# Kernel optimization log

Measured on AMD Instinct MI355X. Metric: run time of the kernel, lower is better.

## Reference

```python
import jax, jax.numpy as jnp
from jax import lax
import numpy as np

V, D_EMB, H, P, B, T = 32000, 512, 1024, 512, 32, 512
NUM_LAYERS = 2


def setup_inputs() -> dict:
    key = jax.random.key(0)
    ks = jax.random.split(key, 2 + NUM_LAYERS * 5)
    tokens = jax.random.randint(ks[0], (B, T), 0, V, dtype=jnp.int32)
    embed = jax.random.normal(ks[1], (V, D_EMB), dtype=jnp.float32) * 0.02
    inp = {"tokens": tokens, "embed": embed}
    in_dims = [D_EMB] + [P] * (NUM_LAYERS - 1)
    for l in range(NUM_LAYERS):
        kk = ks[2 + 5 * l: 7 + 5 * l]
        inp[f"Wx{l}"] = jax.random.normal(kk[0], (in_dims[l], 4 * H), dtype=jnp.float32) * 0.02
        inp[f"Wh{l}"] = jax.random.normal(kk[1], (H, 4 * H), dtype=jnp.float32) * 0.02
        inp[f"b{l}"] = jnp.zeros((4 * H,), dtype=jnp.float32)
        inp[f"Wfc{l}"] = jax.random.normal(kk[3], (H, P), dtype=jnp.float32) * 0.02
        inp[f"bfc{l}"] = jnp.zeros((P,), dtype=jnp.float32)
    return inp


def _lstm(x, Wx, Wh, b):
    # x: [B, T, D] -> [B, T, H]. Keras gate order: i, f, g(cell), o.
    Bsz = x.shape[0]
    h0 = jnp.zeros((Bsz, H), dtype=x.dtype)
    c0 = jnp.zeros((Bsz, H), dtype=x.dtype)

    # Precompute input projection for all timesteps (one big GEMM).
    xz = jnp.einsum('btd,dg->btg', x, Wx) + b  # [B, T, 4H]

    def step(carry, zt):
        h, c = carry
        z = zt + h @ Wh
        i, f, g, o = jnp.split(z, 4, axis=-1)
        c = jax.nn.sigmoid(f) * c + jax.nn.sigmoid(i) * jnp.tanh(g)
        h = jax.nn.sigmoid(o) * jnp.tanh(c)
        return (h, c), h

    _, ys = lax.scan(step, (h0, c0), jnp.swapaxes(xz, 0, 1))  # ys: [T, B, H]
    return jnp.swapaxes(ys, 0, 1)


def reference(tokens, embed, Wx0, Wh0, b0, Wfc0, bfc0, Wx1, Wh1, b1, Wfc1, bfc1):
    # inference path: dropout is identity (training=False), use_softmax=False
    x = embed[tokens]  # [B, T, D_EMB]
    layers = [(Wx0, Wh0, b0, Wfc0, bfc0), (Wx1, Wh1, b1, Wfc1, bfc1)]
    for Wx, Wh, b, Wfc, bfc in layers:
        x = _lstm(x, Wx, Wh, b)
        x = x @ Wfc + bfc  # per-layer dense projection [B, T, P]
    return x
```

## Files before the change

kernel.cpp:

```cpp
#include <hip/hip_runtime.h>
#include <cstdio>
#include <cstdint>

typedef unsigned short u16;
typedef unsigned int u32;
typedef float f32x4 __attribute__((ext_vector_type(4)));
typedef short s16x8 __attribute__((ext_vector_type(8)));
typedef int i32x2 __attribute__((ext_vector_type(2)));

#define DI __device__ __forceinline__

#define BATCH 32
#define SEQT 512
#define HDIM 1024
#define PDIM 512
#define DEMB 512
#define G4H 4096

DI u16 f2bf(float f) {
  u32 u = __float_as_uint(f);
  return (u16)((u + 0x7fffu + ((u >> 16) & 1u)) >> 16);
}
DI float bf2f(u16 h) { return __uint_as_float(((u32)h) << 16); }
DI void split2(float f, u16 &hi, u16 &lo) {
  hi = f2bf(f);
  lo = f2bf(f - bf2f(hi));
}
DI f32x4 mfma16(s16x8 a, s16x8 b, f32x4 c) {
  return __builtin_amdgcn_mfma_f32_16x16x32_bf16(a, b, c, 0, 0, 0);
}
DI void dma16(const void *g, void *l) {
  __builtin_amdgcn_global_load_lds((const __attribute__((address_space(1))) void *)g,
                                   (__attribute__((address_space(3))) void *)l, 16, 0, 0);
}
DI s16x8 ld128_dev(const u16 *p) {
  s16x8 r;
  asm volatile("global_load_dwordx4 %0, %1, off sc1" : "=v"(r) : "v"(p));
  return r;
}
DI i32x2 ld64_dev(const u16 *p) {
  i32x2 r;
  asm volatile("global_load_dwordx2 %0, %1, off sc1" : "=v"(r) : "v"(p));
  return r;
}
DI void st16_dev(u16 *p, u16 v) {
  asm volatile("global_store_short %0, %1, off sc1" ::"v"(p), "v"((u32)v) : "memory");
}
DI void st32_dev(int *p, int v) {
  asm volatile("global_store_dword %0, %1, off sc1" ::"v"(p), "v"(v) : "memory");
}
DI void st64_dev(u16 *p, i32x2 v) {
  asm volatile("global_store_dwordx2 %0, %1, off sc1" ::"v"(p), "v"(v) : "memory");
}
DI u32 sentq(s16x8 v) {
  union U { s16x8 s; u32 d[4]; } u;
  u.s = v;
  u32 b = 0;
#pragma unroll
  for (int i = 0; i < 4; ++i)
    b |= (u32)(((u.d[i] & 0xffffu) == 0xffffu) || ((u.d[i] >> 16) == 0xffffu));
  return b;
}

#if __has_builtin(__builtin_amdgcn_exp2f) && __has_builtin(__builtin_amdgcn_rcpf)
DI float fsig(float x) {
  return __builtin_amdgcn_rcpf(1.f + __builtin_amdgcn_exp2f(-1.4426950408889634f * x));
}
DI float ftanh(float x) {
  return 2.f * __builtin_amdgcn_rcpf(1.f + __builtin_amdgcn_exp2f(-2.8853900817779268f * x)) - 1.f;
}
#else
DI float fsig(float x) { return 1.f / (1.f + expf(-x)); }
DI float ftanh(float x) { return tanhf(x); }
#endif

__global__ void k_gather_pack(const int *__restrict__ tokens, const float *__restrict__ embed,
                              u16 *__restrict__ xhi, u16 *__restrict__ xlo) {
  int idx = blockIdx.x * 256 + threadIdx.x;
  int m = idx >> 6;
  int k8 = (idx & 63) << 3;
  int tok = tokens[m];
  const float *src = embed + (size_t)tok * DEMB + k8;
  float4 a = *(const float4 *)src;
  float4 b = *(const float4 *)(src + 4);
  float v[8] = {a.x, a.y, a.z, a.w, b.x, b.y, b.z, b.w};
  union UV { u16 h[8]; int4 v; };
  UV uh, ul;
#pragma unroll
  for (int j = 0; j < 8; ++j) split2(v[j], uh.h[j], ul.h[j]);
  size_t o = (size_t)m * DEMB + k8;
  *(int4 *)(xhi + o) = uh.v;
  *(int4 *)(xlo + o) = ul.v;
}

__global__ void k_packT(const float *__restrict__ W, u16 *__restrict__ Thi, u16 *__restrict__ Tlo,
                        int K, int N) {
  __shared__ float tile[32][33];
  int n0 = blockIdx.x * 32, k0 = blockIdx.y * 32;
  int tx = threadIdx.x, ty = threadIdx.y;
#pragma unroll
  for (int i = 0; i < 4; ++i) tile[ty + 8 * i][tx] = W[(size_t)(k0 + ty + 8 * i) * N + n0 + tx];
  __syncthreads();
#pragma unroll
  for (int i = 0; i < 4; ++i) {
    int n = ty + 8 * i;
    u16 hi, lo;
    split2(tile[tx][n], hi, lo);
    size_t o = (size_t)(n0 + n) * K + k0 + tx;
    Thi[o] = hi;
    Tlo[o] = lo;
  }
}

__global__ void k_split(const float *__restrict__ W, u16 *__restrict__ hi, u16 *__restrict__ lo,
                        int n) {
  int i = blockIdx.x * 256 + threadIdx.x;
  if (i < n) split2(W[i], hi[i], lo[i]);
}

__global__ void k_beff(const float *__restrict__ bfc0, const float *__restrict__ Wx1,
                       const float *__restrict__ b1, float *__restrict__ beff) {
  int n = blockIdx.x * 256 + threadIdx.x;
  float acc = b1[n];
  for (int j = 0; j < PDIM; ++j) acc += bfc0[j] * Wx1[(size_t)j * G4H + n];
  beff[n] = acc;
}

template <int OM, int SA>
__global__ __launch_bounds__(256, 2) void k_gemm(const u16 *__restrict__ Ahi, const u16 *__restrict__ Alo,
                                                 const u16 *__restrict__ Bhi, const u16 *__restrict__ Blo,
                                                 const float *__restrict__ bias, void *__restrict__ out0,
                                                 int M, int N, int K) {
  __shared__ u16 sP[4][128 * 64];
  const int tid = threadIdx.x;
  const int w = tid >> 6, lane = tid & 63;
  const int la15 = lane & 15, la4 = lane >> 4;
  const int nbn = N >> 7;
  const int bm = blockIdx.x / nbn, bn = blockIdx.x % nbn;
  const u16 *src = (w == 0) ? Ahi : (w == 1) ? Alo : (w == 2) ? Bhi : Blo;
  const int rowbase = (w < 2) ? bm * 128 : bn * 128;
  char *lds = (char *)&sP[w][0];

  if (SA) {
    for (int i = tid; i < 2048; i += 256) ((unsigned long long *)&sP[1][0])[i] = 0ULL;
  }

  f32x4 acc[2][8] = {};
  for (int kb = 0; kb < K; kb += 64) {
    if (!(SA && w == 1)) {
#pragma unroll
      for (int i = 0; i < 16; ++i) {
        int s = i * 64 + lane;
        int row = s >> 3;
        int k16 = (s & 7) ^ (row & 7);
        dma16(src + (size_t)(rowbase + row) * K + kb + k16 * 8, lds + i * 1024);
      }
    }
    asm volatile("s_waitcnt vmcnt(0)" ::: "memory");
    __syncthreads();
#pragma unroll
    for (int ksl = 0; ksl < 2; ++ksl) {
      s16x8 ah[2], al[2];
#pragma unroll
      for (int rf = 0; rf < 2; ++rf) {
        int row = 32 * w + 16 * rf + la15;
        int slot = row * 8 + ((4 * ksl + la4) ^ (row & 7));
        ah[rf] = *(const s16x8 *)((const char *)&sP[0][0] + slot * 16);
        al[rf] = *(const s16x8 *)((const char *)&sP[1][0] + slot * 16);
      }
#pragma unroll
      for (int cf = 0; cf < 8; ++cf) {
        int col = 16 * cf + la15;
        int slot = col * 8 + ((4 * ksl + la4) ^ (col & 7));
        s16x8 bh = *(const s16x8 *)((const char *)&sP[2][0] + slot * 16);
        s16x8 bl = *(const s16x8 *)((const char *)&sP[3][0] + slot * 16);
#pragma unroll
        for (int rf = 0; rf < 2; ++rf) {
          acc[rf][cf] = mfma16(ah[rf], bh, acc[rf][cf]);
          acc[rf][cf] = mfma16(ah[rf], bl, acc[rf][cf]);
          acc[rf][cf] = mfma16(al[rf], bh, acc[rf][cf]);
        }
      }
    }
    __syncthreads();
  }
#pragma unroll
  for (int rf = 0; rf < 2; ++rf) {
#pragma unroll
    for (int cf = 0; cf < 8; ++cf) {
      int c = bn * 128 + 16 * cf + la15;
      float bv = bias ? bias[c] : 0.f;
#pragma unroll
      for (int q = 0; q < 4; ++q) {
        int r = bm * 128 + 32 * w + 16 * rf + 4 * la4 + q;
        float v = acc[rf][cf][q] + bv;
        if (OM == 0) {
          ((u16 *)out0)[(size_t)r * N + c] = f2bf(v);
        } else {
          int b2 = r & 31, tt = r >> 5;
          ((float *)out0)[((size_t)b2 * SEQT + tt) * PDIM + c] = v;
        }
      }
    }
  }
}

__global__ __launch_bounds__(256, 1) void k_recur_pipe(
    const u16 *__restrict__ xz0, const float *__restrict__ Wh0, const float *__restrict__ Wh1,
    const u16 *__restrict__ Weff, const float *__restrict__ beff,
    u16 *h0h, u16 *h1h, u16 *zeffR, int *flags) {
  __shared__ u16 sW[32 * 1024];
  __shared__ u16 sE[32 * 1024];
  __shared__ float zacc[4][32][33];
  __shared__ float zE[32][33];
  __shared__ float sC[256];
  const int tid = threadIdx.x;
  const int w = tid >> 6, lane = tid & 63;
  const int la15 = lane & 15, la4 = lane >> 4;
  const int wg = blockIdx.x;
  const int layer = wg >> 7;
  const int g = wg & 127;

  const float *Wh = layer ? Wh1 : Wh0;
  for (int i2 = tid; i2 < 32 * 1024; i2 += 256) {
    int zc = i2 & 31;
    int k = i2 >> 5;
    int gcol = (zc >> 3) * HDIM + 8 * g + (zc & 7);
    int boff = zc * 2048 + ((((k >> 3) ^ (zc & 7))) << 4) + (k & 7) * 2;
    *(u16 *)((char *)sW + boff) = f2bf(Wh[(size_t)k * G4H + gcol]);
    if (!layer) *(u16 *)((char *)sE + boff) = Weff[(size_t)k * G4H + gcol];
  }
  sC[tid] = 0.f;
  __syncthreads();

  const int r_g = tid >> 3, hc = tid & 7;
  const int ks0 = 8 * w;

  if (!layer) {
    for (int t = 0; t <= SEQT; ++t) {
      const bool last = (t == SEQT);
      float xzv[4] = {0.f, 0.f, 0.f, 0.f};
      if (!last) {
        const u16 *px = xz0 + ((size_t)r_g * SEQT + t) * G4H + 8 * g + hc;
#pragma unroll
        for (int gi = 0; gi < 4; ++gi) xzv[gi] = bf2f(px[(size_t)gi * HDIM]);
      }
      if (w == 0 && (t & 7) == 0 && t >= 16) {
        const int *f1 = flags + 128 + lane;
        const int bp = t - 9;
        for (long tries = 0;; ++tries) {
          int c = __hip_atomic_load(f1, __ATOMIC_RELAXED, __HIP_MEMORY_SCOPE_AGENT);
          int d = __hip_atomic_load(f1 + 64, __ATOMIC_RELAXED, __HIP_MEMORY_SCOPE_AGENT);
          if (__all(c >= bp && d >= bp)) break;
          if (tries > (1L << 22)) break;
          __builtin_amdgcn_s_sleep(1);
        }
      }
      if (t > 0) {
        const u16 *pA = h0h + (size_t)(t - 1) * 32 * HDIM;
        s16x8 aw0[8], aw1[8];
        for (long tries = 0;; ++tries) {
#pragma unroll
          for (int j8 = 0; j8 < 8; ++j8)
            aw0[j8] = ld128_dev(pA + (size_t)la15 * HDIM + 32 * (ks0 + j8) + 8 * la4);
#pragma unroll
          for (int j8 = 0; j8 < 8; ++j8)
            aw1[j8] = ld128_dev(pA + (size_t)(16 + la15) * HDIM + 32 * (ks0 + j8) + 8 * la4);
          asm volatile("s_waitcnt vmcnt(0)" ::: "memory");
          __builtin_amdgcn_sched_barrier(0);
          u32 bad = 0;
#pragma unroll
          for (int j8 = 0; j8 < 8; ++j8) bad |= sentq(aw0[j8]) | sentq(aw1[j8]);
          if (__all(bad == 0)) break;
          if (tries > (1L << 17)) break;
          __builtin_amdgcn_s_sleep(2);
        }
        u16 *zb = zeffR + ((((size_t)((t - 1) & 15) * 128 + g) << 12) + (w << 10));
#pragma unroll
        for (int rt = 0; rt < 2; ++rt) {
          f32x4 acc0[2] = {}, accE[2] = {};
#pragma unroll
          for (int j8 = 0; j8 < 8; ++j8) {
            s16x8 a = rt ? aw1[j8] : aw0[j8];
#pragma unroll
            for (int cf = 0; cf < 2; ++cf) {
              int zc = 16 * cf + la15;
              int sl = (4 * (ks0 + j8) + la4) ^ (zc & 7);
              int boff = zc * 2048 + (sl << 4);
              if (!last) acc0[cf] = mfma16(a, *(const s16x8 *)((const char *)sW + boff), acc0[cf]);
              accE[cf] = mfma16(a, *(const s16x8 *)((const char *)sE + boff), accE[cf]);
            }
          }
#pragma unroll
          for (int cf = 0; cf < 2; ++cf) {
            if (!last) {
#pragma unroll
              for (int q = 0; q < 4; ++q)
                zacc[w][16 * rt + 4 * la4 + q][16 * cf + la15] = acc0[cf][q];
            }
            i32x2 pk;
            pk[0] = (int)(((u32)f2bf(accE[cf][1]) << 16) | (u32)f2bf(accE[cf][0]));
            pk[1] = (int)(((u32)f2bf(accE[cf][3]) << 16) | (u32)f2bf(accE[cf][2]));
            st64_dev(zb + ((rt * 2 + cf) << 8) + (lane << 2), pk);
          }
        }
      }
      __syncthreads();
      if (!last) {
        float z4[4];
#pragma unroll
        for (int gi = 0; gi < 4; ++gi) {
          float s = xzv[gi];
          if (t > 0) {
            int zc = gi * 8 + hc;
            s += zacc[0][r_g][zc] + zacc[1][r_g][zc] + zacc[2][r_g][zc] + zacc[3][r_g][zc];
          }
          z4[gi] = s;
        }
        float ig = fsig(z4[0]);
        float fg = fsig(z4[1]);
        float gg = ftanh(z4[2]);
        float og = fsig(z4[3]);
        float c = fg * sC[tid] + ig * gg;
        sC[tid] = c;
        float h = og * ftanh(c);
        st16_dev(h0h + ((size_t)t * 32 + r_g) * HDIM + 8 * g + hc, f2bf(h));
      }
      asm volatile("s_waitcnt vmcnt(0)" ::: "memory");
      __syncthreads();
      if (tid == 0) st32_dev(flags + g, t + 1);
    }
  } else {
    float bef[4];
#pragma unroll
    for (int gi = 0; gi < 4; ++gi) bef[gi] = beff[gi * HDIM + 8 * g + hc];
    const int rtL = w >> 1, cfL = w & 1;
    for (int t = 0; t < SEQT; ++t) {
      s16x8 aw0[8], aw1[8];
      const u16 *pA = h1h + ((t > 0) ? (size_t)(t - 1) * 32 * HDIM : 0);
      if (t > 0) {
#pragma unroll
        for (int j8 = 0; j8 < 8; ++j8)
          aw0[j8] = ld128_dev(pA + (size_t)la15 * HDIM + 32 * (ks0 + j8) + 8 * la4);
#pragma unroll
        for (int j8 = 0; j8 < 8; ++j8)
          aw1[j8] = ld128_dev(pA + (size_t)(16 + la15) * HDIM + 32 * (ks0 + j8) + 8 * la4);
      }
      {
        const int *f0 = flags + lane;
        const int need0 = t + 2;
        for (long tries = 0;; ++tries) {
          int a = __hip_atomic_load(f0, __ATOMIC_RELAXED, __HIP_MEMORY_SCOPE_AGENT);
          int b = __hip_atomic_load(f0 + 64, __ATOMIC_RELAXED, __HIP_MEMORY_SCOPE_AGENT);
          if (__all(a >= need0 && b >= need0)) break;
          if (tries > (1L << 22)) break;
          __builtin_amdgcn_s_sleep(1);
        }
      }
      const u16 *rb = zeffR + ((((size_t)(t & 15) * 128 + g) << 12) + (w << 8) + (lane << 2));
      i32x2 zp0 = ld64_dev(rb);
      i32x2 zp1 = ld64_dev(rb + 1024);
      i32x2 zp2 = ld64_dev(rb + 2048);
      i32x2 zp3 = ld64_dev(rb + 3072);
      asm volatile("s_waitcnt vmcnt(0)" ::: "memory");
      __builtin_amdgcn_sched_barrier(0);
      {
        float s0 = bf2f((u16)((u32)zp0[0] & 0xffffu)) + bf2f((u16)((u32)zp1[0] & 0xffffu)) +
                   bf2f((u16)((u32)zp2[0] & 0xffffu)) + bf2f((u16)((u32)zp3[0] & 0xffffu));
        float s1 = bf2f((u16)((u32)zp0[0] >> 16)) + bf2f((u16)((u32)zp1[0] >> 16)) +
                   bf2f((u16)((u32)zp2[0] >> 16)) + bf2f((u16)((u32)zp3[0] >> 16));
        float s2 = bf2f((u16)((u32)zp0[1] & 0xffffu)) + bf2f((u16)((u32)zp1[1] & 0xffffu)) +
                   bf2f((u16)((u32)zp2[1] & 0xffffu)) + bf2f((u16)((u32)zp3[1] & 0xffffu));
        float s3 = bf2f((u16)((u32)zp0[1] >> 16)) + bf2f((u16)((u32)zp1[1] >> 16)) +
                   bf2f((u16)((u32)zp2[1] >> 16)) + bf2f((u16)((u32)zp3[1] >> 16));
        int zcL = 16 * cfL + la15, rowL = 16 * rtL + 4 * la4;
        zE[rowL + 0][zcL] = s0;
        zE[rowL + 1][zcL] = s1;
        zE[rowL + 2][zcL] = s2;
        zE[rowL + 3][zcL] = s3;
      }
      if (t > 0) {
        for (long tries = 0;; ++tries) {
          u32 bad = 0;
#pragma unroll
          for (int j8 = 0; j8 < 8; ++j8) bad |= sentq(aw0[j8]) | sentq(aw1[j8]);
          if (__all(bad == 0)) break;
          if (tries > (1L << 17)) break;
          __builtin_amdgcn_s_sleep(2);
#pragma unroll
          for (int j8 = 0; j8 < 8; ++j8)
            aw0[j8] = ld128_dev(pA + (size_t)la15 * HDIM + 32 * (ks0 + j8) + 8 * la4);
#pragma unroll
          for (int j8 = 0; j8 < 8; ++j8)
            aw1[j8] = ld128_dev(pA + (size_t)(16 + la15) * HDIM + 32 * (ks0 + j8) + 8 * la4);
          asm volatile("s_waitcnt vmcnt(0)" ::: "memory");
          __builtin_amdgcn_sched_barrier(0);
        }
#pragma unroll
        for (int rt = 0; rt < 2; ++rt) {
          f32x4 acc0[2] = {};
#pragma unroll
          for (int j8 = 0; j8 < 8; ++j8) {
            s16x8 a = rt ? aw1[j8] : aw0[j8];
#pragma unroll
            for (int cf = 0; cf < 2; ++cf) {
              int zc = 16 * cf + la15;
              int sl = (4 * (ks0 + j8) + la4) ^ (zc & 7);
              int boff = zc * 2048 + (sl << 4);
              acc0[cf] = mfma16(a, *(const s16x8 *)((const char *)sW + boff), acc0[cf]);
            }
          }
#pragma unroll
          for (int cf = 0; cf < 2; ++cf)
#pragma unroll
            for (int q = 0; q < 4; ++q)
              zacc[w][16 * rt + 4 * la4 + q][16 * cf + la15] = acc0[cf][q];
        }
      }
      __syncthreads();
      if (tid == 0) st32_dev(flags + 128 + g, t + 1);
      {
        float z4[4];
#pragma unroll
        for (int gi = 0; gi < 4; ++gi) {
          int zc = gi * 8 + hc;
          float s = bef[gi] + zE[r_g][zc];
          if (t > 0)
            s += zacc[0][r_g][zc] + zacc[1][r_g][zc] + zacc[2][r_g][zc] + zacc[3][r_g][zc];
          z4[gi] = s;
        }
        float ig = fsig(z4[0]);
        float fg = fsig(z4[1]);
        float gg = ftanh(z4[2]);
        float og = fsig(z4[3]);
        float c = fg * sC[tid] + ig * gg;
        sC[tid] = c;
        float h = og * ftanh(c);
        st16_dev(h1h + ((size_t)t * 32 + r_g) * HDIM + 8 * g + hc, f2bf(h));
      }
      __syncthreads();
    }
  }
}

extern "C" void kernel_launch(void *const *d_in, const int *in_sizes, int n_in,
                              void *d_out, int out_size, void *d_ws, size_t ws_size,
                              hipStream_t stream) {
  const int *tokens = (const int *)d_in[0];
  const float *embed = (const float *)d_in[1];
  const float *Wx0 = (const float *)d_in[2];
  const float *Wh0 = (const float *)d_in[3];
  const float *b0 = (const float *)d_in[4];
  const float *Wfc0 = (const float *)d_in[5];
  const float *bfc0 = (const float *)d_in[6];
  const float *Wx1 = (const float *)d_in[7];
  const float *Wh1 = (const float *)d_in[8];
  const float *b1 = (const float *)d_in[9];
  const float *Wfc1 = (const float *)d_in[10];
  const float *bfc1 = (const float *)d_in[11];

  constexpr size_t NEED = 255856640;
  if (ws_size < NEED) {
    fprintf(stderr, "RNNLM kernel: ws too small (%zu < %zu)\n", ws_size, NEED);
    return;
  }
  char *ws = (char *)d_ws;
  u16 *xz0 = (u16 *)(ws + 0);
  u16 *h0h = (u16 *)(ws + 134217728);
  u16 *h1h = (u16 *)(ws + 167772160);
  u16 *x0hi = (u16 *)(ws + 201326592);
  u16 *x0lo = (u16 *)(ws + 218103808);
  u16 *Weff = (u16 *)(ws + 201326592);
  u16 *Wfc0hi = (u16 *)(ws + 209715200);
  u16 *Wfc0lo = (u16 *)(ws + 210763776);
  u16 *WfcT1hi = (u16 *)(ws + 211812352);
  u16 *WfcT1lo = (u16 *)(ws + 212860928);
  float *beff = (float *)(ws + 213909504);
  int *flags = (int *)(ws + 213925888);
  u16 *zeffR = (u16 *)(ws + 218103808);
  u16 *WxT0hi = (u16 *)(ws + 234881024);
  u16 *WxT0lo = (u16 *)(ws + 239075328);
  u16 *WxT1hi = (u16 *)(ws + 243269632);
  u16 *WxT1lo = (u16 *)(ws + 247463936);

  (void)hipMemsetAsync(h0h, 0xFF, 67108864, stream);

  k_packT<<<dim3(G4H / 32, DEMB / 32), dim3(32, 8), 0, stream>>>(Wx0, WxT0hi, WxT0lo, DEMB, G4H);
  k_packT<<<dim3(G4H / 32, DEMB / 32), dim3(32, 8), 0, stream>>>(Wx1, WxT1hi, WxT1lo, DEMB, G4H);
  k_gather_pack<<<4096, 256, 0, stream>>>(tokens, embed, x0hi, x0lo);
  k_gemm<0, 0><<<dim3(128 * 32), 256, 0, stream>>>(x0hi, x0lo, WxT0hi, WxT0lo, b0, xz0,
                                                   16384, G4H, DEMB);
  k_split<<<2048, 256, 0, stream>>>(Wfc0, Wfc0hi, Wfc0lo, HDIM * PDIM);
  k_packT<<<dim3(PDIM / 32, HDIM / 32), dim3(32, 8), 0, stream>>>(Wfc1, WfcT1hi, WfcT1lo, HDIM, PDIM);
  k_beff<<<16, 256, 0, stream>>>(bfc0, Wx1, b1, beff);
  (void)hipMemsetAsync(flags, 0, 256 * sizeof(int), stream);
  k_gemm<0, 0><<<dim3(8 * 32), 256, 0, stream>>>(Wfc0hi, Wfc0lo, WxT1hi, WxT1lo, nullptr, Weff,
                                                 1024, G4H, PDIM);
  {
    const u16 *a0 = xz0; const float *a1 = Wh0; const float *a2 = Wh1;
    const u16 *a3 = Weff; const float *a4 = beff;
    u16 *a5 = h0h; u16 *a6 = h1h; u16 *a7 = zeffR; int *a8 = flags;
    void *args[] = {&a0, &a1, &a2, &a3, &a4, &a5, &a6, &a7, &a8};
    hipError_t e = hipLaunchCooperativeKernel((void *)k_recur_pipe, dim3(256), dim3(256), args, 0, stream);
    if (e != hipSuccess) fprintf(stderr, "coop launch failed: %d\n", (int)e);
  }
  k_gemm<2, 1><<<dim3(128 * 4), 256, 0, stream>>>(h1h, h1h, WfcT1hi, WfcT1lo, bfc1, d_out,
                                                  16384, PDIM, HDIM);
}
```

Before: 4.862 ms.

## Split recurrent workgroup into two independent row-group wavefronts, drop block barriers

The recurrent kernel drops from four waves per workgroup, which split K and reduced partial sums through shared memory with __syncthreads, to two waves. Each wave owns 16 batch rows and the full K=1024 reduction, so no cross-wave barrier is needed. Producer/consumer flags become per-wave rather than per-workgroup, and the zeff buffer is repartitioned so each wave exchanges its own partials with the matching layer-1 wave. This removes block-wide syncs and cross-wave reductions from the serial timestep path. In exchange each wave runs twice as many MFMAs serially, loads all of h from global memory itself, and the block has fewer waves to hide latency.

```diff
diff --git a/kernel.cpp b/kernel.cpp
--- a/kernel.cpp
+++ b/kernel.cpp
@@ -42,9 +42,6 @@
   i32x2 r;
   asm volatile("global_load_dwordx2 %0, %1, off sc1" : "=v"(r) : "v"(p));
   return r;
-}
-DI void st16_dev(u16 *p, u16 v) {
-  asm volatile("global_store_short %0, %1, off sc1" ::"v"(p), "v"((u32)v) : "memory");
 }
 DI void st32_dev(int *p, int v) {
   asm volatile("global_store_dword %0, %1, off sc1" ::"v"(p), "v"(v) : "memory");
@@ -205,24 +202,22 @@
   }
 }
 
-__global__ __launch_bounds__(256, 1) void k_recur_pipe(
+__global__ __launch_bounds__(128, 1) void k_recur_pipe(
     const u16 *__restrict__ xz0, const float *__restrict__ Wh0, const float *__restrict__ Wh1,
     const u16 *__restrict__ Weff, const float *__restrict__ beff,
     u16 *h0h, u16 *h1h, u16 *zeffR, int *flags) {
   __shared__ u16 sW[32 * 1024];
   __shared__ u16 sE[32 * 1024];
-  __shared__ float zacc[4][32][33];
-  __shared__ float zE[32][33];
-  __shared__ float sC[256];
+  __shared__ float zex[2][16][33];
   const int tid = threadIdx.x;
-  const int w = tid >> 6, lane = tid & 63;
+  const int rg = tid >> 6, lane = tid & 63;
   const int la15 = lane & 15, la4 = lane >> 4;
   const int wg = blockIdx.x;
   const int layer = wg >> 7;
   const int g = wg & 127;
 
   const float *Wh = layer ? Wh1 : Wh0;
-  for (int i2 = tid; i2 < 32 * 1024; i2 += 256) {
+  for (int i2 = tid; i2 < 32 * 1024; i2 += 128) {
     int zc = i2 & 31;
     int k = i2 >> 5;
     int gcol = (zc >> 3) * HDIM + 8 * g + (zc & 7);
@@ -230,215 +225,188 @@
     *(u16 *)((char *)sW + boff) = f2bf(Wh[(size_t)k * G4H + gcol]);
     if (!layer) *(u16 *)((char *)sE + boff) = Weff[(size_t)k * G4H + gcol];
   }
-  sC[tid] = 0.f;
   __syncthreads();
 
-  const int r_g = tid >> 3, hc = tid & 7;
-  const int ks0 = 8 * w;
+  const int lrow = lane >> 2, c0 = (lane & 3) * 2;
+  const int grow = 16 * rg + lrow;
+  const int fid = g * 2 + rg;
+  float cst[2] = {0.f, 0.f};
 
   if (!layer) {
     for (int t = 0; t <= SEQT; ++t) {
       const bool last = (t == SEQT);
-      float xzv[4] = {0.f, 0.f, 0.f, 0.f};
+      float xzv[2][4];
       if (!last) {
-        const u16 *px = xz0 + ((size_t)r_g * SEQT + t) * G4H + 8 * g + hc;
-#pragma unroll
-        for (int gi = 0; gi < 4; ++gi) xzv[gi] = bf2f(px[(size_t)gi * HDIM]);
-      }
-      if (w == 0 && (t & 7) == 0 && t >= 16) {
-        const int *f1 = flags + 128 + lane;
+        const u16 *px = xz0 + ((size_t)grow * SEQT + t) * G4H + 8 * g;
+#pragma unroll
+        for (int ci = 0; ci < 2; ++ci)
+#pragma unroll
+          for (int gi = 0; gi < 4; ++gi) xzv[ci][gi] = bf2f(px[gi * HDIM + c0 + ci]);
+      }
+      if ((t & 7) == 0 && t >= 16) {
+        const int *f1 = flags + 256 + fid;
         const int bp = t - 9;
         for (long tries = 0;; ++tries) {
-          int c = __hip_atomic_load(f1, __ATOMIC_RELAXED, __HIP_MEMORY_SCOPE_AGENT);
-          int d = __hip_atomic_load(f1 + 64, __ATOMIC_RELAXED, __HIP_MEMORY_SCOPE_AGENT);
-          if (__all(c >= bp && d >= bp)) break;
+          int v = __hip_atomic_load(f1, __ATOMIC_RELAXED, __HIP_MEMORY_SCOPE_AGENT);
+          if (v >= bp) break;
           if (tries > (1L << 22)) break;
           __builtin_amdgcn_s_sleep(1);
         }
       }
       if (t > 0) {
-        const u16 *pA = h0h + (size_t)(t - 1) * 32 * HDIM;
-        s16x8 aw0[8], aw1[8];
-        for (long tries = 0;; ++tries) {
-#pragma unroll
-          for (int j8 = 0; j8 < 8; ++j8)
-            aw0[j8] = ld128_dev(pA + (size_t)la15 * HDIM + 32 * (ks0 + j8) + 8 * la4);
-#pragma unroll
-          for (int j8 = 0; j8 < 8; ++j8)
-            aw1[j8] = ld128_dev(pA + (size_t)(16 + la15) * HDIM + 32 * (ks0 + j8) + 8 * la4);
-          asm volatile("s_waitcnt vmcnt(0)" ::: "memory");
-          __builtin_amdgcn_sched_barrier(0);
-          u32 bad = 0;
-#pragma unroll
-          for (int j8 = 0; j8 < 8; ++j8) bad |= sentq(aw0[j8]) | sentq(aw1[j8]);
-          if (__all(bad == 0)) break;
-          if (tries > (1L << 17)) break;
-          __builtin_amdgcn_s_sleep(2);
-        }
-        u16 *zb = zeffR + ((((size_t)((t - 1) & 15) * 128 + g) << 12) + (w << 10));
-#pragma unroll
-        for (int rt = 0; rt < 2; ++rt) {
-          f32x4 acc0[2] = {}, accE[2] = {};
-#pragma unroll
-          for (int j8 = 0; j8 < 8; ++j8) {
-            s16x8 a = rt ? aw1[j8] : aw0[j8];
+        const u16 *pA = h0h + ((size_t)(t - 1) * 32 + 16 * rg) * HDIM;
+        f32x4 accW[2] = {}, accE[2] = {};
+#pragma unroll
+        for (int ph = 0; ph < 2; ++ph) {
+          s16x8 aw[16];
+          for (long tries = 0;; ++tries) {
+#pragma unroll
+            for (int i = 0; i < 16; ++i)
+              aw[i] = ld128_dev(pA + (size_t)la15 * HDIM + 512 * ph + 32 * i + 8 * la4);
+            asm volatile("s_waitcnt vmcnt(0)" ::: "memory");
+            __builtin_amdgcn_sched_barrier(0);
+            u32 bad = 0;
+#pragma unroll
+            for (int i = 0; i < 16; ++i) bad |= sentq(aw[i]);
+            if (__all(bad == 0)) break;
+            if (tries > (1L << 17)) break;
+            __builtin_amdgcn_s_sleep(2);
+          }
+#pragma unroll
+          for (int i = 0; i < 16; ++i) {
 #pragma unroll
             for (int cf = 0; cf < 2; ++cf) {
               int zc = 16 * cf + la15;
-              int sl = (4 * (ks0 + j8) + la4) ^ (zc & 7);
+              int sl = (4 * (16 * ph + i) + la4) ^ (zc & 7);
               int boff = zc * 2048 + (sl << 4);
-              if (!last) acc0[cf] = mfma16(a, *(const s16x8 *)((const char *)sW + boff), acc0[cf]);
-              accE[cf] = mfma16(a, *(const s16x8 *)((const char *)sE + boff), accE[cf]);
+              if (!last) accW[cf] = mfma16(aw[i], *(const s16x8 *)((const char *)sW + boff), accW[cf]);
+              accE[cf] = mfma16(aw[i], *(const s16x8 *)((const char *)sE + boff), accE[cf]);
             }
           }
-#pragma unroll
-          for (int cf = 0; cf < 2; ++cf) {
-            if (!last) {
-#pragma unroll
-              for (int q = 0; q < 4; ++q)
-                zacc[w][16 * rt + 4 * la4 + q][16 * cf + la15] = acc0[cf][q];
+        }
+        u16 *zb = zeffR + (((size_t)((t - 1) & 15) * 256 + fid) << 9);
+#pragma unroll
+        for (int cf = 0; cf < 2; ++cf) {
+          i32x2 pk;
+          pk[0] = (int)(((u32)f2bf(accE[cf][1]) << 16) | (u32)f2bf(accE[cf][0]));
+          pk[1] = (int)(((u32)f2bf(accE[cf][3]) << 16) | (u32)f2bf(accE[cf][2]));
+          st64_dev(zb + (cf << 8) + (lane << 2), pk);
+        }
+        if (!last) {
+#pragma unroll
+          for (int cf = 0; cf < 2; ++cf)
+#pragma unroll
+            for (int q = 0; q < 4; ++q) zex[rg][4 * la4 + q][16 * cf + la15] = accW[cf][q];
+        }
+      }
+      if (!last) {
+        u32 hp = 0;
+#pragma unroll
+        for (int ci = 0; ci < 2; ++ci) {
+          float z4[4];
+#pragma unroll
+          for (int gi = 0; gi < 4; ++gi) {
+            float s = xzv[ci][gi];
+            if (t > 0) s += zex[rg][lrow][gi * 8 + c0 + ci];
+            z4[gi] = s;
+          }
+          float ig = fsig(z4[0]);
+          float fg = fsig(z4[1]);
+          float gg = ftanh(z4[2]);
+          float og = fsig(z4[3]);
+          cst[ci] = fg * cst[ci] + ig * gg;
+          float h = og * ftanh(cst[ci]);
+          hp |= ((u32)f2bf(h)) << (16 * ci);
+        }
+        st32_dev((int *)(h0h + ((size_t)t * 32 + grow) * HDIM + 8 * g + c0), (int)hp);
+      }
+      asm volatile("s_waitcnt vmcnt(0)" ::: "memory");
+      if (lane == 0) st32_dev(flags + fid, t + 1);
+    }
+  } else {
+    float bef[2][4];
+#pragma unroll
+    for (int ci = 0; ci < 2; ++ci)
+#pragma unroll
+      for (int gi = 0; gi < 4; ++gi) bef[ci][gi] = beff[gi * HDIM + 8 * g + c0 + ci];
+    for (int t = 0; t < SEQT; ++t) {
+      {
+        const int *f0 = flags + fid;
+        const int need0 = t + 2;
+        for (long tries = 0;; ++tries) {
+          int v = __hip_atomic_load(f0, __ATOMIC_RELAXED, __HIP_MEMORY_SCOPE_AGENT);
+          if (v >= need0) break;
+          if (tries > (1L << 22)) break;
+          __builtin_amdgcn_s_sleep(1);
+        }
+      }
+      const u16 *rb = zeffR + (((size_t)(t & 15) * 256 + fid) << 9);
+      i32x2 zp0 = ld64_dev(rb + (lane << 2));
+      i32x2 zp1 = ld64_dev(rb + 256 + (lane << 2));
+      asm volatile("s_waitcnt vmcnt(0)" ::: "memory");
+      __builtin_amdgcn_sched_barrier(0);
+      float zf[2][4];
+      zf[0][0] = bf2f((u16)((u32)zp0[0] & 0xffffu));
+      zf[0][1] = bf2f((u16)((u32)zp0[0] >> 16));
+      zf[0][2] = bf2f((u16)((u32)zp0[1] & 0xffffu));
+      zf[0][3] = bf2f((u16)((u32)zp0[1] >> 16));
+      zf[1][0] = bf2f((u16)((u32)zp1[0] & 0xffffu));
+      zf[1][1] = bf2f((u16)((u32)zp1[0] >> 16));
+      zf[1][2] = bf2f((u16)((u32)zp1[1] & 0xffffu));
+      zf[1][3] = bf2f((u16)((u32)zp1[1] >> 16));
+      f32x4 accW[2] = {};
+      if (t > 0) {
+        const u16 *pA = h1h + ((size_t)(t - 1) * 32 + 16 * rg) * HDIM;
+#pragma unroll
+        for (int ph = 0; ph < 2; ++ph) {
+          s16x8 aw[16];
+          for (long tries = 0;; ++tries) {
+#pragma unroll
+            for (int i = 0; i < 16; ++i)
+              aw[i] = ld128_dev(pA + (size_t)la15 * HDIM + 512 * ph + 32 * i + 8 * la4);
+            asm volatile("s_waitcnt vmcnt(0)" ::: "memory");
+            __builtin_amdgcn_sched_barrier(0);
+            u32 bad = 0;
+#pragma unroll
+            for (int i = 0; i < 16; ++i) bad |= sentq(aw[i]);
+            if (__all(bad == 0)) break;
+            if (tries > (1L << 17)) break;
+            __builtin_amdgcn_s_sleep(2);
+          }
+#pragma unroll
+          for (int i = 0; i < 16; ++i) {
+#pragma unroll
+            for (int cf = 0; cf < 2; ++cf) {
+              int zc = 16 * cf + la15;
+              int sl = (4 * (16 * ph + i) + la4) ^ (zc & 7);
+              int boff = zc * 2048 + (sl << 4);
+              accW[cf] = mfma16(aw[i], *(const s16x8 *)((const char *)sW + boff), accW[cf]);
             }
-            i32x2 pk;
-            pk[0] = (int)(((u32)f2bf(accE[cf][1]) << 16) | (u32)f2bf(accE[cf][0]));
-            pk[1] = (int)(((u32)f2bf(accE[cf][3]) << 16) | (u32)f2bf(accE[cf][2]));
-            st64_dev(zb + ((rt * 2 + cf) << 8) + (lane << 2), pk);
           }
         }
       }
-      __syncthreads();
-      if (!last) {
+      if (lane == 0) st32_dev(flags + 256 + fid, t + 1);
+#pragma unroll
+      for (int cf = 0; cf < 2; ++cf)
+#pragma unroll
+        for (int q = 0; q < 4; ++q)
+          zex[rg][4 * la4 + q][16 * cf + la15] = accW[cf][q] + zf[cf][q];
+      u32 hp = 0;
+#pragma unroll
+      for (int ci = 0; ci < 2; ++ci) {
         float z4[4];
 #pragma unroll
-        for (int gi = 0; gi < 4; ++gi) {
-          float s = xzv[gi];
-          if (t > 0) {
-            int zc = gi * 8 + hc;
-            s += zacc[0][r_g][zc] + zacc[1][r_g][zc] + zacc[2][r_g][zc] + zacc[3][r_g][zc];
-          }
-          z4[gi] = s;
-        }
+        for (int gi = 0; gi < 4; ++gi)
+          z4[gi] = bef[ci][gi] + zex[rg][lrow][gi * 8 + c0 + ci];
         float ig = fsig(z4[0]);
         float fg = fsig(z4[1]);
         float gg = ftanh(z4[2]);
         float og = fsig(z4[3]);
-        float c = fg * sC[tid] + ig * gg;
-        sC[tid] = c;
-        float h = og * ftanh(c);
-        st16_dev(h0h + ((size_t)t * 32 + r_g) * HDIM + 8 * g + hc, f2bf(h));
-      }
-      asm volatile("s_waitcnt vmcnt(0)" ::: "memory");
-      __syncthreads();
-      if (tid == 0) st32_dev(flags + g, t + 1);
-    }
-  } else {
-    float bef[4];
-#pragma unroll
-    for (int gi = 0; gi < 4; ++gi) bef[gi] = beff[gi * HDIM + 8 * g + hc];
-    const int rtL = w >> 1, cfL = w & 1;
-    for (int t = 0; t < SEQT; ++t) {
-      s16x8 aw0[8], aw1[8];
-      const u16 *pA = h1h + ((t > 0) ? (size_t)(t - 1) * 32 * HDIM : 0);
-      if (t > 0) {
-#pragma unroll
-        for (int j8 = 0; j8 < 8; ++j8)
-          aw0[j8] = ld128_dev(pA + (size_t)la15 * HDIM + 32 * (ks0 + j8) + 8 * la4);
-#pragma unroll
-        for (int j8 = 0; j8 < 8; ++j8)
-          aw1[j8] = ld128_dev(pA + (size_t)(16 + la15) * HDIM + 32 * (ks0 + j8) + 8 * la4);
-      }
-      {
-        const int *f0 = flags + lane;
-        const int need0 = t + 2;
-        for (long tries = 0;; ++tries) {
-          int a = __hip_atomic_load(f0, __ATOMIC_RELAXED, __HIP_MEMORY_SCOPE_AGENT);
-          int b = __hip_atomic_load(f0 + 64, __ATOMIC_RELAXED, __HIP_MEMORY_SCOPE_AGENT);
-          if (__all(a >= need0 && b >= need0)) break;
-          if (tries > (1L << 22)) break;
-          __builtin_amdgcn_s_sleep(1);
-        }
-      }
-      const u16 *rb = zeffR + ((((size_t)(t & 15) * 128 + g) << 12) + (w << 8) + (lane << 2));
-      i32x2 zp0 = ld64_dev(rb);
-      i32x2 zp1 = ld64_dev(rb + 1024);
-      i32x2 zp2 = ld64_dev(rb + 2048);
-      i32x2 zp3 = ld64_dev(rb + 3072);
-      asm volatile("s_waitcnt vmcnt(0)" ::: "memory");
-      __builtin_amdgcn_sched_barrier(0);
-      {
-        float s0 = bf2f((u16)((u32)zp0[0] & 0xffffu)) + bf2f((u16)((u32)zp1[0] & 0xffffu)) +
-                   bf2f((u16)((u32)zp2[0] & 0xffffu)) + bf2f((u16)((u32)zp3[0] & 0xffffu));
-        float s1 = bf2f((u16)((u32)zp0[0] >> 16)) + bf2f((u16)((u32)zp1[0] >> 16)) +
-                   bf2f((u16)((u32)zp2[0] >> 16)) + bf2f((u16)((u32)zp3[0] >> 16));
-        float s2 = bf2f((u16)((u32)zp0[1] & 0xffffu)) + bf2f((u16)((u32)zp1[1] & 0xffffu)) +
-                   bf2f((u16)((u32)zp2[1] & 0xffffu)) + bf2f((u16)((u32)zp3[1] & 0xffffu));
-        float s3 = bf2f((u16)((u32)zp0[1] >> 16)) + bf2f((u16)((u32)zp1[1] >> 16)) +
-                   bf2f((u16)((u32)zp2[1] >> 16)) + bf2f((u16)((u32)zp3[1] >> 16));
-        int zcL = 16 * cfL + la15, rowL = 16 * rtL + 4 * la4;
-        zE[rowL + 0][zcL] = s0;
-        zE[rowL + 1][zcL] = s1;
-        zE[rowL + 2][zcL] = s2;
-        zE[rowL + 3][zcL] = s3;
-      }
-      if (t > 0) {
-        for (long tries = 0;; ++tries) {
-          u32 bad = 0;
-#pragma unroll
-          for (int j8 = 0; j8 < 8; ++j8) bad |= sentq(aw0[j8]) | sentq(aw1[j8]);
-          if (__all(bad == 0)) break;
-          if (tries > (1L << 17)) break;
-          __builtin_amdgcn_s_sleep(2);
-#pragma unroll
-          for (int j8 = 0; j8 < 8; ++j8)
-            aw0[j8] = ld128_dev(pA + (size_t)la15 * HDIM + 32 * (ks0 + j8) + 8 * la4);
-#pragma unroll
-          for (int j8 = 0; j8 < 8; ++j8)
-            aw1[j8] = ld128_dev(pA + (size_t)(16 + la15) * HDIM + 32 * (ks0 + j8) + 8 * la4);
-          asm volatile("s_waitcnt vmcnt(0)" ::: "memory");
-          __builtin_amdgcn_sched_barrier(0);
-        }
-#pragma unroll
-        for (int rt = 0; rt < 2; ++rt) {
-          f32x4 acc0[2] = {};
-#pragma unroll
-          for (int j8 = 0; j8 < 8; ++j8) {
-            s16x8 a = rt ? aw1[j8] : aw0[j8];
-#pragma unroll
-            for (int cf = 0; cf < 2; ++cf) {
-              int zc = 16 * cf + la15;
-              int sl = (4 * (ks0 + j8) + la4) ^ (zc & 7);
-              int boff = zc * 2048 + (sl << 4);
-              acc0[cf] = mfma16(a, *(const s16x8 *)((const char *)sW + boff), acc0[cf]);
-            }
-          }
-#pragma unroll
-          for (int cf = 0; cf < 2; ++cf)
-#pragma unroll
-            for (int q = 0; q < 4; ++q)
-              zacc[w][16 * rt + 4 * la4 + q][16 * cf + la15] = acc0[cf][q];
-        }
-      }
-      __syncthreads();
-      if (tid == 0) st32_dev(flags + 128 + g, t + 1);
-      {
-        float z4[4];
-#pragma unroll
-        for (int gi = 0; gi < 4; ++gi) {
-          int zc = gi * 8 + hc;
-          float s = bef[gi] + zE[r_g][zc];
-          if (t > 0)
-            s += zacc[0][r_g][zc] + zacc[1][r_g][zc] + zacc[2][r_g][zc] + zacc[3][r_g][zc];
-          z4[gi] = s;
-        }
-        float ig = fsig(z4[0]);
-        float fg = fsig(z4[1]);
-        float gg = ftanh(z4[2]);
-        float og = fsig(z4[3]);
-        float c = fg * sC[tid] + ig * gg;
-        sC[tid] = c;
-        float h = og * ftanh(c);
-        st16_dev(h1h + ((size_t)t * 32 + r_g) * HDIM + 8 * g + hc, f2bf(h));
-      }
-      __syncthreads();
+        cst[ci] = fg * cst[ci] + ig * gg;
+        float h = og * ftanh(cst[ci]);
+        hp |= ((u32)f2bf(h)) << (16 * ci);
+      }
+      st32_dev((int *)(h1h + ((size_t)t * 32 + grow) * HDIM + 8 * g + c0), (int)hp);
     }
   }
 }
@@ -493,7 +461,7 @@
   k_split<<<2048, 256, 0, stream>>>(Wfc0, Wfc0hi, Wfc0lo, HDIM * PDIM);
   k_packT<<<dim3(PDIM / 32, HDIM / 32), dim3(32, 8), 0, stream>>>(Wfc1, WfcT1hi, WfcT1lo, HDIM, PDIM);
   k_beff<<<16, 256, 0, stream>>>(bfc0, Wx1, b1, beff);
-  (void)hipMemsetAsync(flags, 0, 256 * sizeof(int), stream);
+  (void)hipMemsetAsync(flags, 0, 512 * sizeof(int), stream);
   k_gemm<0, 0><<<dim3(8 * 32), 256, 0, stream>>>(Wfc0hi, Wfc0lo, WxT1hi, WxT1lo, nullptr, Weff,
                                                  1024, G4H, PDIM);
   {
@@ -501,7 +469,7 @@
     const u16 *a3 = Weff; const float *a4 = beff;
     u16 *a5 = h0h; u16 *a6 = h1h; u16 *a7 = zeffR; int *a8 = flags;
     void *args[] = {&a0, &a1, &a2, &a3, &a4, &a5, &a6, &a7, &a8};
-    hipError_t e = hipLaunchCooperativeKernel((void *)k_recur_pipe, dim3(256), dim3(256), args, 0, stream);
+    hipError_t e = hipLaunchCooperativeKernel((void *)k_recur_pipe, dim3(256), dim3(128), args, 0, stream);
     if (e != hipSuccess) fprintf(stderr, "coop launch failed: %d\n", (int)e);
   }
   k_gemm<2, 1><<<dim3(128 * 4), 256, 0, stream>>>(h1h, h1h, WfcT1hi, WfcT1lo, bfc1, d_out,
```

New measurement: 6.836 ms. 40.6% more time.
